# Optimization experiments

Measured on AMD Instinct MI355X. Metric: run time of the kernel, lower is better.

Reference implementation:

```python
import jax, jax.numpy as jnp
import numpy as np

H = 384
W = 384
C_X = 64       # channels of x (== out_channels)
C_PTX = 64     # channels of ptx
C_IN = C_X + C_PTX  # Linear in_channels = 128
C_OUT = 64
N_TGT = 120000  # number of target pixels (CSR segments)
DEG = 8         # points per target pixel
N_PTS = N_TGT * DEG


def setup_inputs() -> dict:
    key = jax.random.key(0)
    k1, k2, k3, k4 = jax.random.split(key, 4)
    x = jax.random.normal(k1, (1, C_X, H, W), jnp.float32)
    ptx = jax.random.normal(k2, (N_PTS, C_PTX), jnp.float32)
    # CSR row pointer over points per target pixel (monotone, ends at N_PTS)
    point_key = jnp.arange(N_TGT + 1, dtype=jnp.int32) * DEG
    # unique target-pixel indices into H*W
    pixel_tgt_idx = jnp.arange(N_TGT, dtype=jnp.int32)
    sm_w = jax.random.normal(k3, (C_IN, 1), jnp.float32) * 0.05
    sm_b = jnp.zeros((1,), jnp.float32)
    fo_w = jax.random.normal(k4, (C_IN, C_OUT), jnp.float32) * 0.05
    fo_b = jnp.zeros((C_OUT,), jnp.float32)
    return {"x": x, "ptx": ptx, "sm_w": sm_w, "sm_b": sm_b,
            "fo_w": fo_w, "fo_b": fo_b, "point_key": point_key,
            "pixel_tgt_idx": pixel_tgt_idx, "bs": 1, "height": H, "width": W}


def reference(x, ptx, sm_w, sm_b, fo_w, fo_b, point_key, pixel_tgt_idx, bs, height, width):
    # segment id per point from CSR rowptr (static total length for jit)
    seg = jnp.repeat(jnp.arange(N_TGT, dtype=jnp.int32), jnp.diff(point_key),
                     total_repeat_length=N_PTS)
    # pixel features gathered to target pixels, then CSR-gathered to points
    feat_px = x.transpose(0, 2, 3, 1).reshape(height * width, C_X)[pixel_tgt_idx]
    feat = jnp.concatenate([ptx, feat_px[seg]], axis=1)  # [N_PTS, C_IN]
    # _net_forward: identity (base class)
    # segment softmax over points within each pixel group
    logits = feat @ sm_w + sm_b  # [N_PTS, 1]
    m = jax.ops.segment_max(logits, seg, num_segments=N_TGT)
    e = jnp.exp(logits - m[seg])
    s = jax.ops.segment_sum(e, seg, num_segments=N_TGT)
    weight = e / (s[seg] + 1e-16)
    # feat_out projection replaces ptx
    ptx_out = feat @ fo_w + fo_b  # [N_PTS, C_OUT]
    agg = jax.ops.segment_sum(weight * ptx_out, seg, num_segments=N_TGT)  # [N_TGT, C_OUT]
    # list_to_map: scatter aggregated features back to image grid + mask
    flat = jnp.zeros((height * width, C_OUT), x.dtype).at[pixel_tgt_idx].set(agg)
    mask = jnp.zeros((height * width, 1), x.dtype).at[pixel_tgt_idx].set(1.0)
    fmap = flat.reshape(1, height, width, C_OUT).transpose(0, 3, 1, 2)
    mmap = mask.reshape(1, height, width, 1).transpose(0, 3, 1, 2)
    x_out = jnp.where(mmap > 0, fmap, x)
    return x_out, ptx_out
```

## Files before the change

kernel.cpp:

```cpp
#include <hip/hip_runtime.h>
#include <hip/hip_bf16.h>
#include <math.h>

typedef __attribute__((ext_vector_type(8))) short short8v;
typedef __attribute__((ext_vector_type(4))) float float4v;

#define TB 64

__device__ __forceinline__ short f2bf(float f) {
    __hip_bfloat16 h = __float2bfloat16(f);
    short s; __builtin_memcpy(&s, &h, sizeof(short));
    return s;
}
__device__ __forceinline__ float4v mfma_bf16(short8v a, short8v b, float4v c) {
    return __builtin_amdgcn_mfma_f32_16x16x32_bf16(a, b, c, 0, 0, 0);
}

__device__ __forceinline__ int WTI(int row, int col) {
    return row * 72 + (col ^ (((row >> 2) & 7) << 3));
}

__global__ __launch_bounds__(256)
void copy_x_kernel(const float4* __restrict__ x, float4* __restrict__ out, int n4) {
    int i = blockIdx.x * blockDim.x + threadIdx.x;
    if (i < n4) out[i] = x[i];
}

__global__ __launch_bounds__(256, 4)
void fused_kernel(const float* __restrict__ x,
                  const float* __restrict__ ptx,
                  const float* __restrict__ sm_w,
                  const float* __restrict__ fo_w,
                  const float* __restrict__ fo_b,
                  const int* __restrict__ point_key,
                  const int* __restrict__ pixel_tgt_idx,
                  float* __restrict__ xout,
                  float* __restrict__ ptx_out,
                  int n_tgt, int n_pts, int hw)
{
    __shared__ __align__(16) char sraw[34816];
    unsigned short (*fpx)[72] = (unsigned short (*)[72])sraw;
    unsigned short* wTf       = (unsigned short*)(sraw + 9216);
    float (*q_lds)[68]        = (float (*)[68])sraw;
    float (*agg)[68]          = (float (*)[68])(sraw + 17408);
    __shared__ int pix_s[TB], r0_s[TB], deg_s[TB];

    const int tid  = threadIdx.x;
    const int lane = tid & 63;
    const int w    = tid >> 6;
    const int lo16 = lane & 15;
    const int g    = lane >> 4;
    const int t0   = blockIdx.x * TB;
    const int tw0  = w * 16;

    float4 wv[8];
    {
        const float4* fw4 = (const float4*)fo_w;
        #pragma unroll
        for (int i = 0; i < 8; ++i) wv[i] = fw4[i * 256 + tid];
    }
    if (tid < TB) {
        int t = t0 + tid;
        bool v = t < n_tgt;
        int r0 = v ? point_key[t] : 0;
        int d  = v ? (point_key[t + 1] - r0) : 0;
        pix_s[tid] = v ? pixel_tgt_idx[t] : 0;
        r0_s[tid]  = r0;
        deg_s[tid] = d > 8 ? 8 : d;
    }
    float fb[4];
    #pragma unroll
    for (int ct = 0; ct < 4; ++ct) fb[ct] = fo_b[ct * 16 + lo16];

    #pragma unroll
    for (int i = 0; i < 8; ++i) {
        int flat = (i * 256 + tid) * 4;
        int k = flat >> 6, c = flat & 63;
        int wrow0 = (k & 64) + c;
        int col = k & 63;
        wTf[WTI(wrow0 + 0, col)] = (unsigned short)f2bf(wv[i].x);
        wTf[WTI(wrow0 + 1, col)] = (unsigned short)f2bf(wv[i].y);
        wTf[WTI(wrow0 + 2, col)] = (unsigned short)f2bf(wv[i].z);
        wTf[WTI(wrow0 + 3, col)] = (unsigned short)f2bf(wv[i].w);
    }
    __syncthreads();

    int pgm[8];
    #pragma unroll
    for (int mt = 0; mt < 8; ++mt) {
        int tlA = tw0 + mt * 2 + (lo16 >> 3);
        int pg  = r0_s[tlA] + (lo16 & 7);
        pgm[mt] = pg < n_pts ? pg : n_pts - 1;
    }

    {
        const int tgt = tid >> 2, q4 = tid & 3;
        const int pix = pix_s[tgt];
        const float* xp = x + (size_t)(q4 * 16) * hw + pix;
        #pragma unroll
        for (int hhalf = 0; hhalf < 2; ++hhalf) {
            short8v pk;
            #pragma unroll
            for (int j = 0; j < 8; ++j)
                pk[j] = f2bf(xp[(size_t)(hhalf * 8 + j) * hw]);
            *(short8v*)&fpx[tgt][q4 * 16 + hhalf * 8] = pk;
        }
    }

    short8v b1[5][2];
    #pragma unroll
    for (int ct = 0; ct < 4; ++ct)
        #pragma unroll
        for (int kh = 0; kh < 2; ++kh)
            b1[ct][kh] = *(const short8v*)&wTf[WTI(ct * 16 + lo16, kh * 32 + g * 8)];
    #pragma unroll
    for (int kh = 0; kh < 2; ++kh) {
        short8v bb;
        #pragma unroll
        for (int j = 0; j < 8; ++j)
            bb[j] = f2bf(sm_w[kh * 32 + g * 8 + j]);
        b1[4][kh] = bb;
    }

    float4 lb0, lb1, lb2, lb3;
    {
        const float* prow = ptx + (size_t)pgm[0] * 64 + g * 8;
        lb0 = *(const float4*)(prow);
        lb1 = *(const float4*)(prow + 4);
        lb2 = *(const float4*)(prow + 32);
        lb3 = *(const float4*)(prow + 36);
    }
    __syncthreads();

    float4v qv4[4];
    {
        short8v a20 = *(const short8v*)&fpx[tw0 + lo16][g * 8];
        short8v a21 = *(const short8v*)&fpx[tw0 + lo16][32 + g * 8];
        #pragma unroll
        for (int ct = 0; ct < 4; ++ct) {
            short8v b20 = *(const short8v*)&wTf[WTI(64 + ct * 16 + lo16, g * 8)];
            short8v b21 = *(const short8v*)&wTf[WTI(64 + ct * 16 + lo16, 32 + g * 8)];
            float4v z = {0.f, 0.f, 0.f, 0.f};
            z = mfma_bf16(a20, b20, z);
            qv4[ct] = mfma_bf16(a21, b21, z);
        }
    }
    __syncthreads();
    #pragma unroll
    for (int ct = 0; ct < 4; ++ct)
        #pragma unroll
        for (int r = 0; r < 4; ++r)
            q_lds[tw0 + g * 4 + r][ct * 16 + lo16] = qv4[ct][r] + fb[ct];

    auto EPIL = [&](int mt, float4v e0, float4v e1, float4v e2, float4v e3, float4v e4) {
        const int tE   = tw0 + mt * 2 + (g >> 1);
        const int degE = deg_s[tE];
        const int r0E  = r0_s[tE];
        float lgt[4];
        #pragma unroll
        for (int r = 0; r < 4; ++r)
            lgt[r] = (((g & 1) * 4 + r) < degE) ? e4[r] : -3.4e38f;
        float m4 = fmaxf(fmaxf(lgt[0], lgt[1]), fmaxf(lgt[2], lgt[3]));
        float m8 = fmaxf(m4, __shfl_xor(m4, 16));
        float wgt[4], wsum = 0.f;
        #pragma unroll
        for (int r = 0; r < 4; ++r) {
            int pE = (g & 1) * 4 + r;
            wgt[r] = (pE < degE) ? __expf(lgt[r] - m8) : 0.0f;
            wsum += wgt[r];
        }
        wsum += __shfl_xor(wsum, 16);
        const float inv = 1.0f / (wsum + 1e-16f);
        #pragma unroll
        for (int ct = 0; ct < 4; ++ct) {
            float4v ec = (ct == 0) ? e0 : (ct == 1) ? e1 : (ct == 2) ? e2 : e3;
            const int col = ct * 16 + lo16;
            const float qv = q_lds[tE][col];
            float ap = 0.f;
            #pragma unroll
            for (int r = 0; r < 4; ++r) {
                float po = ec[r] + qv;
                int pE = (g & 1) * 4 + r;
                if (pE < degE)
                    ptx_out[(size_t)(r0E + pE) * 64 + col] = po;
                ap = fmaf(wgt[r] * inv, po, ap);
            }
            ap += __shfl_xor(ap, 16);
            if (!(lane & 16)) agg[tE][col] = ap;
        }
    };

    float4v p0, p1, p2, p3, p4;
    #pragma unroll
    for (int mt = 0; mt < 8; ++mt) {
        short8v a0, a1;
        a0[0] = f2bf(lb0.x); a0[1] = f2bf(lb0.y); a0[2] = f2bf(lb0.z); a0[3] = f2bf(lb0.w);
        a0[4] = f2bf(lb1.x); a0[5] = f2bf(lb1.y); a0[6] = f2bf(lb1.z); a0[7] = f2bf(lb1.w);
        a1[0] = f2bf(lb2.x); a1[1] = f2bf(lb2.y); a1[2] = f2bf(lb2.z); a1[3] = f2bf(lb2.w);
        a1[4] = f2bf(lb3.x); a1[5] = f2bf(lb3.y); a1[6] = f2bf(lb3.z); a1[7] = f2bf(lb3.w);

        if (mt < 7) {
            const float* prow = ptx + (size_t)pgm[mt + 1] * 64 + g * 8;
            lb0 = *(const float4*)(prow);
            lb1 = *(const float4*)(prow + 4);
            lb2 = *(const float4*)(prow + 32);
            lb3 = *(const float4*)(prow + 36);
        }

        float4v z = {0.f, 0.f, 0.f, 0.f};
        float4v n0 = mfma_bf16(a1, b1[0][1], mfma_bf16(a0, b1[0][0], z));
        float4v n1 = mfma_bf16(a1, b1[1][1], mfma_bf16(a0, b1[1][0], z));
        float4v n2 = mfma_bf16(a1, b1[2][1], mfma_bf16(a0, b1[2][0], z));
        float4v n3 = mfma_bf16(a1, b1[3][1], mfma_bf16(a0, b1[3][0], z));
        float4v n4 = mfma_bf16(a1, b1[4][1], mfma_bf16(a0, b1[4][0], z));

        if (mt > 0) EPIL(mt - 1, p0, p1, p2, p3, p4);
        p0 = n0; p1 = n1; p2 = n2; p3 = n3; p4 = n4;
    }
    EPIL(7, p0, p1, p2, p3, p4);
    __syncthreads();

    {
        const int tgt = tid >> 2, q4 = tid & 3;
        if (t0 + tgt < n_tgt) {
            const int pix = pix_s[tgt];
            float* xp = xout + (size_t)(q4 * 16) * hw + pix;
            #pragma unroll
            for (int u = 0; u < 4; ++u) {
                float4 v = *(const float4*)&agg[tgt][q4 * 16 + u * 4];
                xp[(size_t)(u * 4 + 0) * hw] = v.x;
                xp[(size_t)(u * 4 + 1) * hw] = v.y;
                xp[(size_t)(u * 4 + 2) * hw] = v.z;
                xp[(size_t)(u * 4 + 3) * hw] = v.w;
            }
        }
    }
}

extern "C" void kernel_launch(void* const* d_in, const int* in_sizes, int n_in,
                              void* d_out, int out_size, void* d_ws, size_t ws_size,
                              hipStream_t stream) {
    const float* x             = (const float*)d_in[0];
    const float* ptx           = (const float*)d_in[1];
    const float* sm_w          = (const float*)d_in[2];
    const float* fo_w          = (const float*)d_in[4];
    const float* fo_b          = (const float*)d_in[5];
    const int*   point_key     = (const int*)d_in[6];
    const int*   pixel_tgt_idx = (const int*)d_in[7];

    const int x_elems = in_sizes[0];
    const int hw      = x_elems / 64;
    const int n_tgt   = in_sizes[7];
    const int n_pts   = in_sizes[1] / 64;

    float* xout    = (float*)d_out;
    float* ptx_out = xout + (size_t)x_elems;

    const int n4 = x_elems / 4;
    copy_x_kernel<<<(n4 + 255) / 256, 256, 0, stream>>>(
        (const float4*)x, (float4*)xout, n4);

    const int blocks = (n_tgt + TB - 1) / TB;
    fused_kernel<<<blocks, 256, 0, stream>>>(
        x, ptx, sm_w, fo_w, fo_b, point_key, pixel_tgt_idx,
        xout, ptx_out, n_tgt, n_pts, hw);
}
```

Measured before the change: 171.2 us.

## Swap MFMA operand order for row-major outputs with vectorized stores and shuffle softmax

```diff
diff --git a/kernel.cpp b/kernel.cpp
--- a/kernel.cpp
+++ b/kernel.cpp
@@ -59,6 +59,10 @@
         #pragma unroll
         for (int i = 0; i < 8; ++i) wv[i] = fw4[i * 256 + tid];
     }
+    float4 fb40 = *(const float4*)&fo_b[ 0 + g * 4];
+    float4 fb41 = *(const float4*)&fo_b[16 + g * 4];
+    float4 fb42 = *(const float4*)&fo_b[32 + g * 4];
+    float4 fb43 = *(const float4*)&fo_b[48 + g * 4];
     if (tid < TB) {
         int t = t0 + tid;
         bool v = t < n_tgt;
@@ -68,9 +72,6 @@
         r0_s[tid]  = r0;
         deg_s[tid] = d > 8 ? 8 : d;
     }
-    float fb[4];
-    #pragma unroll
-    for (int ct = 0; ct < 4; ++ct) fb[ct] = fo_b[ct * 16 + lo16];
 
     #pragma unroll
     for (int i = 0; i < 8; ++i) {
@@ -141,56 +142,44 @@
             short8v b20 = *(const short8v*)&wTf[WTI(64 + ct * 16 + lo16, g * 8)];
             short8v b21 = *(const short8v*)&wTf[WTI(64 + ct * 16 + lo16, 32 + g * 8)];
             float4v z = {0.f, 0.f, 0.f, 0.f};
-            z = mfma_bf16(a20, b20, z);
-            qv4[ct] = mfma_bf16(a21, b21, z);
-        }
-    }
-    __syncthreads();
-    #pragma unroll
-    for (int ct = 0; ct < 4; ++ct)
-        #pragma unroll
-        for (int r = 0; r < 4; ++r)
-            q_lds[tw0 + g * 4 + r][ct * 16 + lo16] = qv4[ct][r] + fb[ct];
-
-    auto EPIL = [&](int mt, float4v e0, float4v e1, float4v e2, float4v e3, float4v e4) {
-        const int tE   = tw0 + mt * 2 + (g >> 1);
-        const int degE = deg_s[tE];
-        const int r0E  = r0_s[tE];
-        float lgt[4];
-        #pragma unroll
-        for (int r = 0; r < 4; ++r)
-            lgt[r] = (((g & 1) * 4 + r) < degE) ? e4[r] : -3.4e38f;
-        float m4 = fmaxf(fmaxf(lgt[0], lgt[1]), fmaxf(lgt[2], lgt[3]));
-        float m8 = fmaxf(m4, __shfl_xor(m4, 16));
-        float wgt[4], wsum = 0.f;
-        #pragma unroll
-        for (int r = 0; r < 4; ++r) {
-            int pE = (g & 1) * 4 + r;
-            wgt[r] = (pE < degE) ? __expf(lgt[r] - m8) : 0.0f;
-            wsum += wgt[r];
-        }
-        wsum += __shfl_xor(wsum, 16);
-        const float inv = 1.0f / (wsum + 1e-16f);
-        #pragma unroll
-        for (int ct = 0; ct < 4; ++ct) {
-            float4v ec = (ct == 0) ? e0 : (ct == 1) ? e1 : (ct == 2) ? e2 : e3;
-            const int col = ct * 16 + lo16;
-            const float qv = q_lds[tE][col];
-            float ap = 0.f;
-            #pragma unroll
-            for (int r = 0; r < 4; ++r) {
-                float po = ec[r] + qv;
-                int pE = (g & 1) * 4 + r;
-                if (pE < degE)
-                    ptx_out[(size_t)(r0E + pE) * 64 + col] = po;
-                ap = fmaf(wgt[r] * inv, po, ap);
-            }
-            ap += __shfl_xor(ap, 16);
-            if (!(lane & 16)) agg[tE][col] = ap;
-        }
-    };
-
-    float4v p0, p1, p2, p3, p4;
+            z = mfma_bf16(b20, a20, z);
+            qv4[ct] = mfma_bf16(b21, a21, z);
+        }
+    }
+    __syncthreads();
+    {
+        float4v t0v = qv4[0]; t0v[0] += fb40.x; t0v[1] += fb40.y; t0v[2] += fb40.z; t0v[3] += fb40.w;
+        float4v t1v = qv4[1]; t1v[0] += fb41.x; t1v[1] += fb41.y; t1v[2] += fb41.z; t1v[3] += fb41.w;
+        float4v t2v = qv4[2]; t2v[0] += fb42.x; t2v[1] += fb42.y; t2v[2] += fb42.z; t2v[3] += fb42.w;
+        float4v t3v = qv4[3]; t3v[0] += fb43.x; t3v[1] += fb43.y; t3v[2] += fb43.z; t3v[3] += fb43.w;
+        *(float4v*)&q_lds[tw0 + lo16][ 0 + g * 4] = t0v;
+        *(float4v*)&q_lds[tw0 + lo16][16 + g * 4] = t1v;
+        *(float4v*)&q_lds[tw0 + lo16][32 + g * 4] = t2v;
+        *(float4v*)&q_lds[tw0 + lo16][48 + g * 4] = t3v;
+    }
+
+#define EPIL_CT(CT, CREG)                                                      \
+    {                                                                          \
+        const int colb = (CT) * 16 + g * 4;                                    \
+        const float4 q4 = *(const float4*)&q_lds[tE][colb];                    \
+        float4v po;                                                            \
+        po[0] = CREG[0] + q4.x; po[1] = CREG[1] + q4.y;                        \
+        po[2] = CREG[2] + q4.z; po[3] = CREG[3] + q4.w;                        \
+        if (val)                                                               \
+            *(float4v*)&ptx_out[(size_t)(r0E + pE) * 64 + colb] = po;          \
+        float s0 = po[0] * wn, s1 = po[1] * wn, s2 = po[2] * wn, s3 = po[3] * wn; \
+        s0 += __shfl_xor(s0, 1); s1 += __shfl_xor(s1, 1);                      \
+        s2 += __shfl_xor(s2, 1); s3 += __shfl_xor(s3, 1);                      \
+        s0 += __shfl_xor(s0, 2); s1 += __shfl_xor(s1, 2);                      \
+        s2 += __shfl_xor(s2, 2); s3 += __shfl_xor(s3, 2);                      \
+        s0 += __shfl_xor(s0, 4); s1 += __shfl_xor(s1, 4);                      \
+        s2 += __shfl_xor(s2, 4); s3 += __shfl_xor(s3, 4);                      \
+        if (pE == 0) {                                                         \
+            float4v ag; ag[0] = s0; ag[1] = s1; ag[2] = s2; ag[3] = s3;        \
+            *(float4v*)&agg[tE][colb] = ag;                                    \
+        }                                                                      \
+    }
+
     #pragma unroll
     for (int mt = 0; mt < 8; ++mt) {
         short8v a0, a1;
@@ -208,16 +197,36 @@
         }
 
         float4v z = {0.f, 0.f, 0.f, 0.f};
-        float4v n0 = mfma_bf16(a1, b1[0][1], mfma_bf16(a0, b1[0][0], z));
-        float4v n1 = mfma_bf16(a1, b1[1][1], mfma_bf16(a0, b1[1][0], z));
-        float4v n2 = mfma_bf16(a1, b1[2][1], mfma_bf16(a0, b1[2][0], z));
-        float4v n3 = mfma_bf16(a1, b1[3][1], mfma_bf16(a0, b1[3][0], z));
-        float4v n4 = mfma_bf16(a1, b1[4][1], mfma_bf16(a0, b1[4][0], z));
-
-        if (mt > 0) EPIL(mt - 1, p0, p1, p2, p3, p4);
-        p0 = n0; p1 = n1; p2 = n2; p3 = n3; p4 = n4;
-    }
-    EPIL(7, p0, p1, p2, p3, p4);
+        float4v cc0 = mfma_bf16(b1[0][1], a1, mfma_bf16(b1[0][0], a0, z));
+        float4v cc1 = mfma_bf16(b1[1][1], a1, mfma_bf16(b1[1][0], a0, z));
+        float4v cc2 = mfma_bf16(b1[2][1], a1, mfma_bf16(b1[2][0], a0, z));
+        float4v cc3 = mfma_bf16(b1[3][1], a1, mfma_bf16(b1[3][0], a0, z));
+        float4v cc4 = mfma_bf16(b1[4][1], a1, mfma_bf16(b1[4][0], a0, z));
+
+        const int tE   = tw0 + mt * 2 + (lo16 >> 3);
+        const int degE = deg_s[tE];
+        const int r0E  = r0_s[tE];
+        const int pE   = lo16 & 7;
+        const bool val = (pE < degE);
+
+        float lg = val ? cc4[0] : -3.4e38f;
+        float mx = lg;
+        mx = fmaxf(mx, __shfl_xor(mx, 1));
+        mx = fmaxf(mx, __shfl_xor(mx, 2));
+        mx = fmaxf(mx, __shfl_xor(mx, 4));
+        float e = val ? __expf(lg - mx) : 0.0f;
+        float sm = e;
+        sm += __shfl_xor(sm, 1);
+        sm += __shfl_xor(sm, 2);
+        sm += __shfl_xor(sm, 4);
+        const float wn = e / (sm + 1e-16f);
+
+        EPIL_CT(0, cc0)
+        EPIL_CT(1, cc1)
+        EPIL_CT(2, cc2)
+        EPIL_CT(3, cc3)
+    }
+#undef EPIL_CT
     __syncthreads();
 
     {
```

Result: faster. 137.0 us (-20.0%).
